# Kernel tuning notes

Hardware: AMD Instinct MI355X
Metric: run time of the kernel (lower is better)

Reference implementation:

```python
import jax, jax.numpy as jnp
import numpy as np

N = 100000   # nodes
E = 1600000  # directed edges
F_IN = 100
H = 256
N_LABELS = 19
BN_EPS = 1e-5


def setup_inputs() -> dict:
    key = jax.random.key(0)
    ks = jax.random.split(key, 12)
    p = lambda k, shape, s=0.05: jax.random.normal(k, shape, dtype=jnp.float32) * s
    return {
        "x": jax.random.normal(ks[0], (N, F_IN), dtype=jnp.float32),
        "edge_index": jax.random.randint(ks[1], (2, E), 0, N, dtype=jnp.int32),
        "W1": p(ks[2], (F_IN, F_IN)), "b1": jnp.zeros((F_IN,), jnp.float32),
        "W2": p(ks[3], (F_IN, F_IN)), "b2": jnp.zeros((F_IN,), jnp.float32),
        "W3": p(ks[4], (F_IN, H)),   "b3": jnp.zeros((H,), jnp.float32),
        "fc1_W": p(ks[5], (H, H)),   "fc1_b": jnp.zeros((H,), jnp.float32),
        "fc2a_W": p(ks[6], (H, 128)), "fc2a_b": jnp.zeros((128,), jnp.float32),
        "bn_gamma": jnp.ones((128,), jnp.float32), "bn_beta": jnp.zeros((128,), jnp.float32),
        "fc2b_W": p(ks[7], (128, N_LABELS)), "fc2b_b": jnp.zeros((N_LABELS,), jnp.float32),
    }


def _gcn_conv(x, W, b, src, dst, dinv):
    """PyG GCNConv with add_self_loops + symmetric normalization.
    out[dst] += dinv[src]*dinv[dst] * (x @ W)[src], plus self-loop term, plus bias.
    """
    n = x.shape[0]
    xw = x @ W  # [N, out]
    norm = dinv[src] * dinv[dst]  # [E]
    agg = jax.ops.segment_sum(xw[src] * norm[:, None], dst, num_segments=n)
    agg = agg + xw * (dinv * dinv)[:, None]  # self loops (i -> i)
    return agg + b


def reference(x, edge_index, W1, b1, W2, b2, W3, b3, fc1_W, fc1_b,
              fc2a_W, fc2a_b, bn_gamma, bn_beta, fc2b_W, fc2b_b):
    src, dst = edge_index[0], edge_index[1]
    n = x.shape[0]
    # degree of augmented graph (A + I), computed on targets (sum aggregation)
    deg = jax.ops.segment_sum(jnp.ones((src.shape[0],), x.dtype), dst, num_segments=n) + 1.0
    dinv = jax.lax.rsqrt(deg)

    h = jnp.clip(x, -0.4, 0.4)
    h = jax.nn.relu(_gcn_conv(h, W1, b1, src, dst, dinv))
    h = jax.nn.relu(_gcn_conv(h, W2, b2, src, dst, dinv))
    h = jax.nn.relu(_gcn_conv(h, W3, b3, src, dst, dinv))
    h = jax.nn.relu(h @ fc1_W + fc1_b)
    # fc2: Linear -> BatchNorm1d (train mode, batch stats) -> ReLU -> Linear
    h = h @ fc2a_W + fc2a_b
    mu = jnp.mean(h, axis=0)
    var = jnp.mean(jnp.square(h - mu), axis=0)  # biased var, as torch BN uses
    h = (h - mu) * jax.lax.rsqrt(var + BN_EPS) * bn_gamma + bn_beta
    h = jax.nn.relu(h)
    logits = h @ fc2b_W + fc2b_b
    return jax.nn.log_softmax(logits, axis=1)
```

## Files before the change

kernel.cpp:

```cpp
#include <hip/hip_runtime.h>
#include <hip/hip_bf16.h>

#define N_NODES 100000
#define N_EDGES 1600000
#define F_IN_DIM 100
#define F_IN_PAD 104
#define H_DIM 256
#define BN_DIM 128
#define N_LABELS 19
#define BN_EPS 1e-5f

#define BUCKET_SHIFT 8
#define NB 391
#define EPB 4096
#define PB 391

typedef __attribute__((ext_vector_type(8))) short bf16x8;
typedef __attribute__((ext_vector_type(4))) short s16x4;
typedef __attribute__((ext_vector_type(4))) float f32x4;

static __device__ inline short f2bf(float f) {
    __hip_bfloat16 h = __float2bfloat16(f);
    return *(short*)&h;
}
static __device__ inline float bf2f(short s) {
    unsigned u = ((unsigned)(unsigned short)s) << 16;
    return __builtin_bit_cast(float, u);
}

__global__ __launch_bounds__(256) void part_hist_kernel(const int* __restrict__ dst,
                                                        int* __restrict__ part_hist, int E)
{
    __shared__ int h[NB];
    int tid = threadIdx.x;
    for (int i = tid; i < NB; i += 256) h[i] = 0;
    __syncthreads();
    int base = blockIdx.x * EPB;
    int end = min(base + EPB, E);
    for (int e = base + tid; e < end; e += 256)
        atomicAdd(&h[dst[e] >> BUCKET_SHIFT], 1);
    __syncthreads();
    for (int i = tid; i < NB; i += 256) part_hist[blockIdx.x * NB + i] = h[i];
}

__global__ __launch_bounds__(512) void bucket_total_kernel(const int* __restrict__ part_hist,
                                                           int* __restrict__ bucket_total)
{
    __shared__ int ls[512];
    int b = blockIdx.x;
    int s = 0;
    for (int p = threadIdx.x; p < PB; p += 512) s += part_hist[p * NB + b];
    ls[threadIdx.x] = s;
    __syncthreads();
    for (int off = 256; off > 0; off >>= 1) {
        if (threadIdx.x < off) ls[threadIdx.x] += ls[threadIdx.x + off];
        __syncthreads();
    }
    if (threadIdx.x == 0) bucket_total[b] = ls[0];
}

__global__ __launch_bounds__(512) void bucket_scan_kernel(const int* __restrict__ bucket_total,
                                                          int* __restrict__ bucket_base)
{
    __shared__ int ls[512];
    int tid = threadIdx.x;
    ls[tid] = (tid < NB) ? bucket_total[tid] : 0;
    __syncthreads();
    for (int off = 1; off < 512; off <<= 1) {
        int v = ls[tid];
        int add = (tid >= off) ? ls[tid - off] : 0;
        __syncthreads();
        ls[tid] = v + add;
        __syncthreads();
    }
    if (tid < NB) bucket_base[tid] = (tid > 0) ? ls[tid - 1] : 0;
    if (tid == 0) bucket_base[NB] = ls[NB - 1];
}

__global__ __launch_bounds__(512) void part_offset_kernel(int* __restrict__ part_hist,
                                                          const int* __restrict__ bucket_base)
{
    __shared__ int ls[512];
    int b = blockIdx.x;
    int tid = threadIdx.x;
    int v = (tid < PB) ? part_hist[tid * NB + b] : 0;
    ls[tid] = v;
    __syncthreads();
    for (int off = 1; off < 512; off <<= 1) {
        int x = ls[tid];
        int add = (tid >= off) ? ls[tid - off] : 0;
        __syncthreads();
        ls[tid] = x + add;
        __syncthreads();
    }
    if (tid < PB) part_hist[tid * NB + b] = bucket_base[b] + ((tid > 0) ? ls[tid - 1] : 0);
}

__global__ __launch_bounds__(256) void partition_kernel(const int* __restrict__ src,
                                                        const int* __restrict__ dst,
                                                        const int* __restrict__ part_hist,
                                                        int* __restrict__ ep, int E)
{
    __shared__ int cur[NB];
    int tid = threadIdx.x;
    for (int i = tid; i < NB; i += 256) cur[i] = part_hist[blockIdx.x * NB + i];
    __syncthreads();
    int base = blockIdx.x * EPB;
    int end = min(base + EPB, E);
    for (int e = base + tid; e < end; e += 256) {
        int d = dst[e];
        int s = src[e];
        int pos = atomicAdd(&cur[d >> BUCKET_SHIFT], 1);
        ep[pos] = (s << 8) | (d & 255);
    }
}

__global__ __launch_bounds__(256) void bucket_csr_kernel(const int* __restrict__ ep,
                                                         const int* __restrict__ bucket_base,
                                                         int* __restrict__ row_start,
                                                         float* __restrict__ dinv,
                                                         int* __restrict__ src_sorted, int N, int E)
{
    __shared__ int h[256], sc[256], cur[256];
    int b = blockIdx.x;
    int tid = threadIdx.x;
    int e0 = bucket_base[b], e1 = bucket_base[b + 1];
    int node0 = b << BUCKET_SHIFT;
    int nn = min(256, N - node0);

    h[tid] = 0;
    __syncthreads();
    for (int e = e0 + tid; e < e1; e += 256)
        atomicAdd(&h[ep[e] & 255], 1);
    __syncthreads();

    sc[tid] = h[tid];
    __syncthreads();
    for (int off = 1; off < 256; off <<= 1) {
        int v = sc[tid];
        int add = (tid >= off) ? sc[tid - off] : 0;
        __syncthreads();
        sc[tid] = v + add;
        __syncthreads();
    }
    int excl = e0 + ((tid > 0) ? sc[tid - 1] : 0);
    if (tid < nn) {
        row_start[node0 + tid] = excl;
        dinv[node0 + tid] = rsqrtf((float)h[tid] + 1.0f);
    }
    cur[tid] = excl;
    __syncthreads();
    for (int e = e0 + tid; e < e1; e += 256) {
        int p = ep[e];
        int pos = atomicAdd(&cur[p & 255], 1);
        src_sorted[pos] = ((unsigned)p) >> 8;
    }
    if (b == 0 && tid == 0) row_start[N] = E;
}

__global__ __launch_bounds__(256) void pack_all(
    const float* __restrict__ W1, const float* __restrict__ W2, const float* __restrict__ W3,
    const float* __restrict__ Wf1, const float* __restrict__ Wf2a,
    short* __restrict__ Wt1, short* __restrict__ Wt2, short* __restrict__ Wt3,
    short* __restrict__ Wtf1, short* __restrict__ Wtf2a)
{
    int idx = blockIdx.x * 256 + threadIdx.x;
    const float* W; short* Wt; int K, N, Kp, local;
    if (idx < 10400)       { W = W1;   Wt = Wt1;   K = 100; N = 100; Kp = 104; local = idx; }
    else if (idx < 20800)  { W = W2;   Wt = Wt2;   K = 100; N = 100; Kp = 104; local = idx - 10400; }
    else if (idx < 47424)  { W = W3;   Wt = Wt3;   K = 100; N = 256; Kp = 104; local = idx - 20800; }
    else if (idx < 112960) { W = Wf1;  Wt = Wtf1;  K = 256; N = 256; Kp = 256; local = idx - 47424; }
    else if (idx < 145728) { W = Wf2a; Wt = Wtf2a; K = 256; N = 128; Kp = 256; local = idx - 112960; }
    else return;
    int n = local / Kp, k = local - n * Kp;
    Wt[local] = (k < K) ? f2bf(W[(size_t)k * N + n]) : (short)0;
}

template<int ABF16>
__global__ __launch_bounds__(256) void gemm_oneshot(
    const void* __restrict__ Av, const short* __restrict__ Wt,
    const float* __restrict__ bias, const float* __restrict__ rowscale,
    short* __restrict__ C, int M, int Nout, int strideA, int strideC, int relu)
{
    __shared__ __align__(16) short As[128][F_IN_PAD];
    __shared__ __align__(16) short Bs[128][F_IN_PAD];
    int tid = threadIdx.x;
    int rowBase = blockIdx.x * 128;
    int colBase = blockIdx.y * 128;

    if (ABF16) {
        const short* A = (const short*)Av;
        for (int ch = tid; ch < 128 * 13; ch += 256) {
            int r = ch / 13, c8 = (ch - r * 13) * 8;
            int gr = rowBase + r;
            bf16x8 o = (bf16x8){0,0,0,0,0,0,0,0};
            if (gr < M) o = *(const bf16x8*)(A + (size_t)gr * strideA + c8);
            *(bf16x8*)(&As[r][c8]) = o;
        }
    } else {
        const float* A = (const float*)Av;
        for (int ch = tid; ch < 128 * 25; ch += 256) {
            int r = ch / 25, c4 = (ch - r * 25) * 4;
            int gr = rowBase + r;
            float4 v = make_float4(0.f, 0.f, 0.f, 0.f);
            if (gr < M) v = *(const float4*)(A + (size_t)gr * strideA + c4);
            v.x = fminf(fmaxf(v.x, -0.4f), 0.4f);
            v.y = fminf(fmaxf(v.y, -0.4f), 0.4f);
            v.z = fminf(fmaxf(v.z, -0.4f), 0.4f);
            v.w = fminf(fmaxf(v.w, -0.4f), 0.4f);
            s16x4 o = (s16x4){f2bf(v.x), f2bf(v.y), f2bf(v.z), f2bf(v.w)};
            *(s16x4*)(&As[r][c4]) = o;
        }
        for (int r = tid; r < 128; r += 256)
            *(s16x4*)(&As[r][100]) = (s16x4){0, 0, 0, 0};
    }
    for (int ch = tid; ch < 128 * 13; ch += 256) {
        int n = ch / 13, c8 = (ch - n * 13) * 8;
        int gn = colBase + n;
        bf16x8 o = (bf16x8){0,0,0,0,0,0,0,0};
        if (gn < Nout) o = *(const bf16x8*)(Wt + (size_t)gn * F_IN_PAD + c8);
        *(bf16x8*)(&Bs[n][c8]) = o;
    }
    __syncthreads();

    int wid = tid >> 6;
    int lane = tid & 63;
    int quad = lane >> 4, l15 = lane & 15;
    int wave_m = (wid & 1) * 64;
    int wave_n = (wid >> 1) * 64;

    f32x4 acc[4][4];
    #pragma unroll
    for (int i = 0; i < 4; i++)
        #pragma unroll
        for (int j = 0; j < 4; j++)
            acc[i][j] = (f32x4){0.f, 0.f, 0.f, 0.f};

    #pragma unroll
    for (int kc = 0; kc < 4; kc++) {
        int off = kc * 32 + quad * 8;
        bool ok = (off + 8 <= F_IN_PAD);
        bf16x8 a[4], b[4];
        #pragma unroll
        for (int im = 0; im < 4; im++)
            a[im] = ok ? *(const bf16x8*)(&As[wave_m + im * 16 + l15][off])
                       : (bf16x8){0,0,0,0,0,0,0,0};
        #pragma unroll
        for (int in = 0; in < 4; in++)
            b[in] = ok ? *(const bf16x8*)(&Bs[wave_n + in * 16 + l15][off])
                       : (bf16x8){0,0,0,0,0,0,0,0};
        #pragma unroll
        for (int im = 0; im < 4; im++)
            #pragma unroll
            for (int in = 0; in < 4; in++)
                acc[im][in] = __builtin_amdgcn_mfma_f32_16x16x32_bf16(
                    a[im], b[in], acc[im][in], 0, 0, 0);
    }

    #pragma unroll
    for (int im = 0; im < 4; im++) {
        #pragma unroll
        for (int reg = 0; reg < 4; reg++) {
            int row = rowBase + wave_m + im * 16 + quad * 4 + reg;
            if (row >= M) continue;
            float rs = rowscale ? rowscale[row] : 1.f;
            #pragma unroll
            for (int in = 0; in < 4; in++) {
                int col = colBase + wave_n + in * 16 + l15;
                if (col >= strideC) continue;
                float v = 0.f;
                if (col < Nout) {
                    v = acc[im][in][reg];
                    if (bias) v += bias[col];
                    v *= rs;
                    if (relu) v = fmaxf(v, 0.f);
                }
                C[(size_t)row * strideC + col] = f2bf(v);
            }
        }
    }
}

#define SAP 72
__global__ __launch_bounds__(256) void gemm_mfma(
    const short* __restrict__ A, const short* __restrict__ Wt,
    const float* __restrict__ bias, const float* __restrict__ rowscale,
    short* __restrict__ C, int M, int Kp, int Nout,
    int strideA, int strideC, int relu)
{
    __shared__ __align__(16) short As[128][SAP];
    __shared__ __align__(16) short Bs[128][SAP];

    int tid = threadIdx.x;
    int wid = tid >> 6;
    int lane = tid & 63;
    int quad = lane >> 4;
    int l15 = lane & 15;
    int wave_m = (wid & 1) * 64;
    int wave_n = (wid >> 1) * 64;
    int rowBase = blockIdx.y * 128;
    int colBase = blockIdx.x * 128;

    f32x4 acc[4][4];
    #pragma unroll
    for (int i = 0; i < 4; i++)
        #pragma unroll
        for (int j = 0; j < 4; j++)
            acc[i][j] = (f32x4){0.f, 0.f, 0.f, 0.f};

    bf16x8 pa[4], pb[4];
    int nIter = (Kp + 63) >> 6;

    auto loadA = [&](int k0) {
        #pragma unroll
        for (int i = 0; i < 4; i++) {
            int ch = tid + i * 256;
            int r = ch >> 3, c8 = (ch & 7) << 3;
            int gr = rowBase + r, gk = k0 + c8;
            bf16x8 o = (bf16x8){0,0,0,0,0,0,0,0};
            if (gr < M && gk < strideA)
                o = *(const bf16x8*)(A + (size_t)gr * strideA + gk);
            pa[i] = o;
        }
    };
    auto loadB = [&](int k0) {
        #pragma unroll
        for (int i = 0; i < 4; i++) {
            int ch = tid + i * 256;
            int n = ch >> 3, c8 = (ch & 7) << 3;
            int gn = colBase + n, gk = k0 + c8;
            bf16x8 o = (bf16x8){0,0,0,0,0,0,0,0};
            if (gn < Nout && gk < Kp)
                o = *(const bf16x8*)(Wt + (size_t)gn * Kp + gk);
            pb[i] = o;
        }
    };
    auto storeAB = [&]() {
        #pragma unroll
        for (int i = 0; i < 4; i++) {
            int ch = tid + i * 256;
            int r = ch >> 3, c8 = (ch & 7) << 3;
            *(bf16x8*)(&As[r][c8]) = pa[i];
            *(bf16x8*)(&Bs[r][c8]) = pb[i];
        }
    };

    loadA(0); loadB(0);
    for (int it = 0; it < nIter; ++it) {
        if (it > 0) __syncthreads();
        storeAB();
        __syncthreads();
        if (it + 1 < nIter) { loadA((it + 1) << 6); loadB((it + 1) << 6); }
        #pragma unroll
        for (int ks = 0; ks < 2; ks++) {
            bf16x8 a[4], b[4];
            #pragma unroll
            for (int im = 0; im < 4; im++)
                a[im] = *(const bf16x8*)(&As[wave_m + im * 16 + l15][quad * 8 + ks * 32]);
            #pragma unroll
            for (int in = 0; in < 4; in++)
                b[in] = *(const bf16x8*)(&Bs[wave_n + in * 16 + l15][quad * 8 + ks * 32]);
            #pragma unroll
            for (int im = 0; im < 4; im++)
                #pragma unroll
                for (int in = 0; in < 4; in++)
                    acc[im][in] = __builtin_amdgcn_mfma_f32_16x16x32_bf16(
                        a[im], b[in], acc[im][in], 0, 0, 0);
        }
    }

    #pragma unroll
    for (int im = 0; im < 4; im++) {
        #pragma unroll
        for (int reg = 0; reg < 4; reg++) {
            int row = rowBase + wave_m + im * 16 + quad * 4 + reg;
            if (row >= M) continue;
            float rs = rowscale ? rowscale[row] : 1.f;
            #pragma unroll
            for (int in = 0; in < 4; in++) {
                int col = colBase + wave_n + in * 16 + l15;
                if (col >= strideC) continue;
                float v = 0.f;
                if (col < Nout) {
                    v = acc[im][in][reg];
                    if (bias) v += bias[col];
                    v *= rs;
                    if (relu) v = fmaxf(v, 0.f);
                }
                C[(size_t)row * strideC + col] = f2bf(v);
            }
        }
    }
}

template<int F, int STRIDE, int T, int MODE>
__global__ void gather_kernel(const short* __restrict__ xws,
                              const int* __restrict__ row_start,
                              const int* __restrict__ src_sorted,
                              const float* __restrict__ dinv,
                              const float* __restrict__ bias,
                              short* __restrict__ out, int n)
{
    constexpr int CHUNKS = STRIDE / 8;
    int group = (blockIdx.x * blockDim.x + threadIdx.x) / T;
    int lane = threadIdx.x % T;
    if (group >= n) return;
    int d = group;
    int e0 = row_start[d], e1 = row_start[d + 1];
    bool active = (lane < CHUNKS);
    int coff = lane * 8;
    float acc[8] = {};
    for (int e = e0; e < e1; e++) {
        int s = src_sorted[e];
        if (active) {
            bf16x8 v = *(const bf16x8*)(xws + (size_t)s * STRIDE + coff);
            #pragma unroll
            for (int j = 0; j < 8; j++) acc[j] += bf2f(v[j]);
        }
    }
    if (active) {
        bf16x8 xv = *(const bf16x8*)(xws + (size_t)d * STRIDE + coff);
        float di = dinv[d];
        bf16x8 o;
        #pragma unroll
        for (int j = 0; j < 8; j++) {
            int col = coff + j;
            float v = 0.f;
            if (col < F) {
                v = di * (acc[j] + bf2f(xv[j]));
                if (MODE == 0) v = fmaxf(v + bias[col], 0.f);
                if (MODE == 1) v = di * fmaxf(v + bias[col], 0.f);
            }
            o[j] = f2bf(v);
        }
        *(bf16x8*)(out + (size_t)d * STRIDE + coff) = o;
    }
}

__global__ void bn_stats_kernel(const short* __restrict__ h,
                                float* __restrict__ sum, float* __restrict__ sumsq, int Ntot)
{
    int c = threadIdx.x & 127;
    int rpb = blockDim.x >> 7;
    int r0 = blockIdx.x * rpb + (threadIdx.x >> 7);
    int stride = gridDim.x * rpb;
    float s = 0.f, ss = 0.f;
    for (int r = r0; r < Ntot; r += stride) {
        float v = bf2f(h[(size_t)r * BN_DIM + c]);
        s += v; ss += v * v;
    }
    __shared__ float ls[256], lss[256];
    ls[threadIdx.x] = s; lss[threadIdx.x] = ss;
    __syncthreads();
    if (threadIdx.x < 128) {
        s = ls[threadIdx.x] + ls[threadIdx.x + 128];
        ss = lss[threadIdx.x] + lss[threadIdx.x + 128];
        atomicAdd(&sum[c], s);
        atomicAdd(&sumsq[c], ss);
    }
}

__global__ void bn_finalize_kernel(const float* __restrict__ sum, const float* __restrict__ sumsq,
                                   const float* __restrict__ gamma, const float* __restrict__ beta,
                                   float* __restrict__ a, float* __restrict__ b, int Ntot)
{
    int c = threadIdx.x;
    float inv_n = 1.0f / (float)Ntot;
    float mu = sum[c] * inv_n;
    float var = sumsq[c] * inv_n - mu * mu;
    float ai = gamma[c] * rsqrtf(var + BN_EPS);
    a[c] = ai;
    b[c] = beta[c] - mu * ai;
}

__global__ __launch_bounds__(256) void fc2b_fused_kernel(
    const short* __restrict__ h, const float* __restrict__ bn_a, const float* __restrict__ bn_b,
    const float* __restrict__ W, const float* __restrict__ bias,
    float* __restrict__ out, int Ntot)
{
    __shared__ float Ws[BN_DIM][N_LABELS + 1];
    __shared__ float as[BN_DIM], bs[BN_DIM];
    for (int i = threadIdx.x; i < BN_DIM * N_LABELS; i += 256) {
        int k = i / N_LABELS, j = i - k * N_LABELS;
        Ws[k][j] = W[i];
    }
    if (threadIdx.x < BN_DIM) {
        as[threadIdx.x] = bn_a[threadIdx.x];
        bs[threadIdx.x] = bn_b[threadIdx.x];
    }
    __syncthreads();

    int r = blockIdx.x * 256 + threadIdx.x;
    if (r >= Ntot) return;

    float acc[N_LABELS];
    #pragma unroll
    for (int j = 0; j < N_LABELS; j++) acc[j] = bias[j];

    const short* hr = h + (size_t)r * BN_DIM;
    #pragma unroll
    for (int k0 = 0; k0 < BN_DIM; k0 += 8) {
        bf16x8 hv = *(const bf16x8*)(hr + k0);
        #pragma unroll
        for (int t = 0; t < 8; t++) {
            float v = fmaxf(bf2f(hv[t]) * as[k0 + t] + bs[k0 + t], 0.f);
            #pragma unroll
            for (int j = 0; j < N_LABELS; j++)
                acc[j] = fmaf(v, Ws[k0 + t][j], acc[j]);
        }
    }

    float m = acc[0];
    #pragma unroll
    for (int j = 1; j < N_LABELS; j++) m = fmaxf(m, acc[j]);
    float s = 0.f;
    #pragma unroll
    for (int j = 0; j < N_LABELS; j++) s += expf(acc[j] - m);
    float lse = m + logf(s);
    float* o = out + (size_t)r * N_LABELS;
    #pragma unroll
    for (int j = 0; j < N_LABELS; j++) o[j] = acc[j] - lse;
}

extern "C" void kernel_launch(void* const* d_in, const int* in_sizes, int n_in,
                              void* d_out, int out_size, void* d_ws, size_t ws_size,
                              hipStream_t stream)
{
    const float* x      = (const float*)d_in[0];
    const int*   ei     = (const int*)d_in[1];
    const float* W1     = (const float*)d_in[2];
    const float* b1     = (const float*)d_in[3];
    const float* W2     = (const float*)d_in[4];
    const float* b2     = (const float*)d_in[5];
    const float* W3     = (const float*)d_in[6];
    const float* b3     = (const float*)d_in[7];
    const float* fc1_W  = (const float*)d_in[8];
    const float* fc1_b  = (const float*)d_in[9];
    const float* fc2aW  = (const float*)d_in[10];
    const float* fc2ab  = (const float*)d_in[11];
    const float* gamma  = (const float*)d_in[12];
    const float* beta   = (const float*)d_in[13];
    const float* fc2bW  = (const float*)d_in[14];
    const float* fc2bb  = (const float*)d_in[15];
    float* out = (float*)d_out;

    const int* src = ei;
    const int* dst = ei + N_EDGES;

    char* w = (char*)d_ws;
    float* dinv        = (float*)w;  w += ((size_t)N_NODES * 4 + 255) / 256 * 256;
    int*   row_start   = (int*)w;    w += ((size_t)(N_NODES + 1) * 4 + 255) / 256 * 256;
    int*   part_hist   = (int*)w;    w += ((size_t)PB * NB * 4 + 255) / 256 * 256;
    int*   bucket_total= (int*)w;    w += ((size_t)NB * 4 + 255) / 256 * 256;
    int*   bucket_base = (int*)w;    w += ((size_t)(NB + 1) * 4 + 255) / 256 * 256;
    float* bn_sum      = (float*)w;  w += 128 * 4;
    float* bn_sumsq    = (float*)w;  w += 128 * 4;
    float* bn_a        = (float*)w;  w += 128 * 4;
    float* bn_b        = (float*)w;  w += 128 * 4;
    short* Wt1         = (short*)w;  w += ((size_t)F_IN_DIM * F_IN_PAD * 2 + 255) / 256 * 256;
    short* Wt2         = (short*)w;  w += ((size_t)F_IN_DIM * F_IN_PAD * 2 + 255) / 256 * 256;
    short* Wt3         = (short*)w;  w += ((size_t)H_DIM * F_IN_PAD * 2 + 255) / 256 * 256;
    short* Wtf1        = (short*)w;  w += ((size_t)H_DIM * H_DIM * 2 + 255) / 256 * 256;
    short* Wtf2a       = (short*)w;  w += ((size_t)BN_DIM * H_DIM * 2 + 255) / 256 * 256;
    int*   src_sorted  = (int*)w;    w += ((size_t)N_EDGES * 4 + 255) / 256 * 256;
    int*   ep          = (int*)w;    w += ((size_t)N_EDGES * 4 + 255) / 256 * 256;
    short* xws100      = (short*)w;  w += ((size_t)N_NODES * F_IN_PAD * 2 + 255) / 256 * 256;
    short* agg100      = (short*)w;  w += ((size_t)N_NODES * F_IN_PAD * 2 + 255) / 256 * 256;
    short* big1        = (short*)w;  w += ((size_t)N_NODES * H_DIM * 2 + 255) / 256 * 256;
    short* big2        = (short*)w;  w += ((size_t)N_NODES * H_DIM * 2 + 255) / 256 * 256;

    part_hist_kernel<<<PB, 256, 0, stream>>>(dst, part_hist, N_EDGES);
    bucket_total_kernel<<<NB, 512, 0, stream>>>(part_hist, bucket_total);
    bucket_scan_kernel<<<1, 512, 0, stream>>>(bucket_total, bucket_base);
    part_offset_kernel<<<NB, 512, 0, stream>>>(part_hist, bucket_base);
    partition_kernel<<<PB, 256, 0, stream>>>(src, dst, part_hist, ep, N_EDGES);
    bucket_csr_kernel<<<NB, 256, 0, stream>>>(ep, bucket_base, row_start, dinv,
                                              src_sorted, N_NODES, N_EDGES);

    pack_all<<<570, 256, 0, stream>>>(W1, W2, W3, fc1_W, fc2aW, Wt1, Wt2, Wt3, Wtf1, Wtf2a);

    const int nOne = (N_NODES + 127) / 128;
    int gatherBlocks = (N_NODES * 16 + 255) / 256;

    gemm_oneshot<0><<<dim3(nOne, 1), 256, 0, stream>>>(
        x, Wt1, nullptr, dinv, xws100, N_NODES, F_IN_DIM, F_IN_DIM, F_IN_PAD, 0);
    gather_kernel<F_IN_DIM, F_IN_PAD, 16, 0><<<gatherBlocks, 256, 0, stream>>>(
        xws100, row_start, src_sorted, dinv, b1, agg100, N_NODES);

    gemm_oneshot<1><<<dim3(nOne, 1), 256, 0, stream>>>(
        agg100, Wt2, nullptr, dinv, xws100, N_NODES, F_IN_DIM, F_IN_PAD, F_IN_PAD, 0);
    gather_kernel<F_IN_DIM, F_IN_PAD, 16, 1><<<gatherBlocks, 256, 0, stream>>>(
        xws100, row_start, src_sorted, dinv, b2, agg100, N_NODES);

    gather_kernel<F_IN_DIM, F_IN_PAD, 16, 2><<<gatherBlocks, 256, 0, stream>>>(
        agg100, row_start, src_sorted, dinv, nullptr, xws100, N_NODES);
    gemm_oneshot<1><<<dim3(nOne, 2), 256, 0, stream>>>(
        xws100, Wt3, b3, nullptr, big1, N_NODES, H_DIM, F_IN_PAD, H_DIM, 1);

    gemm_mfma<<<dim3(2, nOne), 256, 0, stream>>>(
        big1, Wtf1, fc1_b, nullptr, big2, N_NODES, H_DIM, H_DIM, H_DIM, H_DIM, 1);

    gemm_mfma<<<dim3(1, nOne), 256, 0, stream>>>(
        big2, Wtf2a, fc2ab, nullptr, big1, N_NODES, H_DIM, BN_DIM, H_DIM, BN_DIM, 0);

    hipMemsetAsync(bn_sum, 0, 2 * 128 * 4, stream);
    bn_stats_kernel<<<512, 256, 0, stream>>>(big1, bn_sum, bn_sumsq, N_NODES);
    bn_finalize_kernel<<<1, 128, 0, stream>>>(bn_sum, bn_sumsq, gamma, beta, bn_a, bn_b, N_NODES);

    fc2b_fused_kernel<<<(N_NODES + 255) / 256, 256, 0, stream>>>(
        big1, bn_a, bn_b, fc2bW, fc2bb, out, N_NODES);
}
```

Before: 725.3 us.

## Replace pipelined 128x128 GEMM with one-shot K=256 64x64 tile kernel

The two dense layers with K=256 (fc1 and fc2a) now use a new kernel that loads a whole 64-row by 256-K A tile and a 64-column B tile into shared memory in one go. It uses an XOR swizzle to avoid bank conflicts and drops the double-buffered K loop and its repeated barriers. Smaller tiles give more blocks and better occupancy, but A rows are reloaded once per column tile (4x for fc1, 2x for fc2a), so global reads rise. Each wave computes only a 64x16 output slice, which lowers register use but also MFMA work per LDS read.

```diff
diff --git a/kernel.cpp b/kernel.cpp
--- a/kernel.cpp
+++ b/kernel.cpp
@@ -281,114 +281,74 @@
     }
 }
 
-#define SAP 72
-__global__ __launch_bounds__(256) void gemm_mfma(
+__global__ __launch_bounds__(256) void gemm_oneshot256(
     const short* __restrict__ A, const short* __restrict__ Wt,
-    const float* __restrict__ bias, const float* __restrict__ rowscale,
-    short* __restrict__ C, int M, int Kp, int Nout,
-    int strideA, int strideC, int relu)
-{
-    __shared__ __align__(16) short As[128][SAP];
-    __shared__ __align__(16) short Bs[128][SAP];
-
-    int tid = threadIdx.x;
-    int wid = tid >> 6;
+    const float* __restrict__ bias, short* __restrict__ C,
+    int M, int Nout, int strideC, int relu)
+{
+    __shared__ __align__(16) short As[64 * 256];
+    __shared__ __align__(16) short Bs[64 * 256];
+    int tid = threadIdx.x;
+    int rowBase = blockIdx.x * 64;
+    int colBase = blockIdx.y * 64;
+
+    #pragma unroll
+    for (int i = 0; i < 8; i++) {
+        int ch = tid + i * 256;
+        int r = ch >> 5, c = ch & 31;
+        int gr = rowBase + r;
+        bf16x8 o = (bf16x8){0,0,0,0,0,0,0,0};
+        if (gr < M) o = *(const bf16x8*)(A + (size_t)gr * 256 + (c << 3));
+        *(bf16x8*)(&As[(r << 8) + (((c ^ r) & 31) << 3)]) = o;
+    }
+    #pragma unroll
+    for (int i = 0; i < 8; i++) {
+        int ch = tid + i * 256;
+        int n = ch >> 5, c = ch & 31;
+        int gn = colBase + n;
+        bf16x8 o = (bf16x8){0,0,0,0,0,0,0,0};
+        if (gn < Nout) o = *(const bf16x8*)(Wt + (size_t)gn * 256 + (c << 3));
+        *(bf16x8*)(&Bs[(n << 8) + (((c ^ n) & 31) << 3)]) = o;
+    }
+    __syncthreads();
+
+    int wv = tid >> 6;
     int lane = tid & 63;
-    int quad = lane >> 4;
-    int l15 = lane & 15;
-    int wave_m = (wid & 1) * 64;
-    int wave_n = (wid >> 1) * 64;
-    int rowBase = blockIdx.y * 128;
-    int colBase = blockIdx.x * 128;
-
-    f32x4 acc[4][4];
-    #pragma unroll
-    for (int i = 0; i < 4; i++)
-        #pragma unroll
-        for (int j = 0; j < 4; j++)
-            acc[i][j] = (f32x4){0.f, 0.f, 0.f, 0.f};
-
-    bf16x8 pa[4], pb[4];
-    int nIter = (Kp + 63) >> 6;
-
-    auto loadA = [&](int k0) {
-        #pragma unroll
-        for (int i = 0; i < 4; i++) {
-            int ch = tid + i * 256;
-            int r = ch >> 3, c8 = (ch & 7) << 3;
-            int gr = rowBase + r, gk = k0 + c8;
-            bf16x8 o = (bf16x8){0,0,0,0,0,0,0,0};
-            if (gr < M && gk < strideA)
-                o = *(const bf16x8*)(A + (size_t)gr * strideA + gk);
-            pa[i] = o;
-        }
-    };
-    auto loadB = [&](int k0) {
-        #pragma unroll
-        for (int i = 0; i < 4; i++) {
-            int ch = tid + i * 256;
-            int n = ch >> 3, c8 = (ch & 7) << 3;
-            int gn = colBase + n, gk = k0 + c8;
-            bf16x8 o = (bf16x8){0,0,0,0,0,0,0,0};
-            if (gn < Nout && gk < Kp)
-                o = *(const bf16x8*)(Wt + (size_t)gn * Kp + gk);
-            pb[i] = o;
-        }
-    };
-    auto storeAB = [&]() {
-        #pragma unroll
-        for (int i = 0; i < 4; i++) {
-            int ch = tid + i * 256;
-            int r = ch >> 3, c8 = (ch & 7) << 3;
-            *(bf16x8*)(&As[r][c8]) = pa[i];
-            *(bf16x8*)(&Bs[r][c8]) = pb[i];
-        }
-    };
-
-    loadA(0); loadB(0);
-    for (int it = 0; it < nIter; ++it) {
-        if (it > 0) __syncthreads();
-        storeAB();
-        __syncthreads();
-        if (it + 1 < nIter) { loadA((it + 1) << 6); loadB((it + 1) << 6); }
-        #pragma unroll
-        for (int ks = 0; ks < 2; ks++) {
-            bf16x8 a[4], b[4];
-            #pragma unroll
-            for (int im = 0; im < 4; im++)
-                a[im] = *(const bf16x8*)(&As[wave_m + im * 16 + l15][quad * 8 + ks * 32]);
-            #pragma unroll
-            for (int in = 0; in < 4; in++)
-                b[in] = *(const bf16x8*)(&Bs[wave_n + in * 16 + l15][quad * 8 + ks * 32]);
-            #pragma unroll
-            for (int im = 0; im < 4; im++)
-                #pragma unroll
-                for (int in = 0; in < 4; in++)
-                    acc[im][in] = __builtin_amdgcn_mfma_f32_16x16x32_bf16(
-                        a[im], b[in], acc[im][in], 0, 0, 0);
-        }
-    }
-
+    int quad = lane >> 4, l15 = lane & 15;
+    int ncol = wv * 16 + l15;
+
+    f32x4 acc[4];
+    #pragma unroll
+    for (int im = 0; im < 4; im++) acc[im] = (f32x4){0.f, 0.f, 0.f, 0.f};
+
+    #pragma unroll
+    for (int kc = 0; kc < 8; kc++) {
+        int c0 = kc * 4 + quad;
+        bf16x8 b = *(const bf16x8*)(&Bs[(ncol << 8) + (((c0 ^ ncol) & 31) << 3)]);
+        #pragma unroll
+        for (int im = 0; im < 4; im++) {
+            int mrow = im * 16 + l15;
+            bf16x8 a = *(const bf16x8*)(&As[(mrow << 8) + (((c0 ^ mrow) & 31) << 3)]);
+            acc[im] = __builtin_amdgcn_mfma_f32_16x16x32_bf16(a, b, acc[im], 0, 0, 0);
+        }
+    }
+
+    int col = colBase + ncol;
+    bool cvalid = col < Nout;
+    float bv = (bias && cvalid) ? bias[col] : 0.f;
     #pragma unroll
     for (int im = 0; im < 4; im++) {
         #pragma unroll
         for (int reg = 0; reg < 4; reg++) {
-            int row = rowBase + wave_m + im * 16 + quad * 4 + reg;
+            int row = rowBase + im * 16 + quad * 4 + reg;
             if (row >= M) continue;
-            float rs = rowscale ? rowscale[row] : 1.f;
-            #pragma unroll
-            for (int in = 0; in < 4; in++) {
-                int col = colBase + wave_n + in * 16 + l15;
-                if (col >= strideC) continue;
-                float v = 0.f;
-                if (col < Nout) {
-                    v = acc[im][in][reg];
-                    if (bias) v += bias[col];
-                    v *= rs;
-                    if (relu) v = fmaxf(v, 0.f);
-                }
+            float v = 0.f;
+            if (cvalid) {
+                v = acc[im][reg] + bv;
+                if (relu) v = fmaxf(v, 0.f);
+            }
+            if (col < strideC)
                 C[(size_t)row * strideC + col] = f2bf(v);
-            }
         }
     }
 }
@@ -580,6 +540,7 @@
     pack_all<<<570, 256, 0, stream>>>(W1, W2, W3, fc1_W, fc2aW, Wt1, Wt2, Wt3, Wtf1, Wtf2a);
 
     const int nOne = (N_NODES + 127) / 128;
+    const int n64  = (N_NODES + 63) / 64;
     int gatherBlocks = (N_NODES * 16 + 255) / 256;
 
     gemm_oneshot<0><<<dim3(nOne, 1), 256, 0, stream>>>(
@@ -597,11 +558,11 @@
     gemm_oneshot<1><<<dim3(nOne, 2), 256, 0, stream>>>(
         xws100, Wt3, b3, nullptr, big1, N_NODES, H_DIM, F_IN_PAD, H_DIM, 1);
 
-    gemm_mfma<<<dim3(2, nOne), 256, 0, stream>>>(
-        big1, Wtf1, fc1_b, nullptr, big2, N_NODES, H_DIM, H_DIM, H_DIM, H_DIM, 1);
-
-    gemm_mfma<<<dim3(1, nOne), 256, 0, stream>>>(
-        big2, Wtf2a, fc2ab, nullptr, big1, N_NODES, H_DIM, BN_DIM, H_DIM, BN_DIM, 0);
+    gemm_oneshot256<<<dim3(n64, 4), 256, 0, stream>>>(
+        big1, Wtf1, fc1_b, big2, N_NODES, H_DIM, H_DIM, 1);
+
+    gemm_oneshot256<<<dim3(n64, 2), 256, 0, stream>>>(
+        big2, Wtf2a, fc2ab, big1, N_NODES, BN_DIM, BN_DIM, 0);
 
     hipMemsetAsync(bn_sum, 0, 2 * 128 * 4, stream);
     bn_stats_kernel<<<512, 256, 0, stream>>>(big1, bn_sum, bn_sumsq, N_NODES);
```

New measurement: 759.6 us. 4.7% more time.

## Add one-shot full-K MFMA GEMM for fc1 and unroll gather edge loop by two

Applied to the files above, without the earlier changes.

Adds a gemm_oneshot256 kernel that loads a full 64x256 A tile and a 64x256 weight tile into XOR-swizzled LDS once, then runs all K steps with 16x16x32 bf16 MFMA and no K-loop synchronisation. fc1 now uses it instead of the tiled gemm_mfma kernel. This removes per-K-tile barriers and may help LDS bank conflicts, but uses 64KB of LDS per block, which can limit occupancy, and reloads A once per column block. Separately, the gather loop processes two edges per iteration so that more independent loads are in flight.

```diff
diff --git a/kernel.cpp b/kernel.cpp
--- a/kernel.cpp
+++ b/kernel.cpp
@@ -281,6 +281,78 @@
     }
 }
 
+__global__ __launch_bounds__(256) void gemm_oneshot256(
+    const short* __restrict__ A, const short* __restrict__ Wt,
+    const float* __restrict__ bias, short* __restrict__ C,
+    int M, int Nout, int strideC, int relu)
+{
+    __shared__ __align__(16) short As[64 * 256];
+    __shared__ __align__(16) short Bs[64 * 256];
+    int tid = threadIdx.x;
+    int rowBase = blockIdx.y * 64;
+    int colBase = blockIdx.x * 64;
+
+    #pragma unroll
+    for (int i = 0; i < 8; i++) {
+        int ch = tid + i * 256;
+        int r = ch >> 5, c = ch & 31;
+        int gr = rowBase + r;
+        bf16x8 o = (bf16x8){0,0,0,0,0,0,0,0};
+        if (gr < M) o = *(const bf16x8*)(A + (size_t)gr * 256 + (c << 3));
+        *(bf16x8*)(&As[(r << 8) + (((c ^ r) & 31) << 3)]) = o;
+    }
+    #pragma unroll
+    for (int i = 0; i < 8; i++) {
+        int ch = tid + i * 256;
+        int n = ch >> 5, c = ch & 31;
+        int gn = colBase + n;
+        bf16x8 o = (bf16x8){0,0,0,0,0,0,0,0};
+        if (gn < Nout) o = *(const bf16x8*)(Wt + (size_t)gn * 256 + (c << 3));
+        *(bf16x8*)(&Bs[(n << 8) + (((c ^ n) & 31) << 3)]) = o;
+    }
+    __syncthreads();
+
+    int wv = tid >> 6;
+    int lane = tid & 63;
+    int quad = lane >> 4, l15 = lane & 15;
+    int ncol = wv * 16 + l15;
+
+    f32x4 acc[4];
+    #pragma unroll
+    for (int im = 0; im < 4; im++) acc[im] = (f32x4){0.f, 0.f, 0.f, 0.f};
+
+    #pragma unroll
+    for (int kc = 0; kc < 8; kc++) {
+        int c0 = kc * 4 + quad;
+        bf16x8 b = *(const bf16x8*)(&Bs[(ncol << 8) + (((c0 ^ ncol) & 31) << 3)]);
+        #pragma unroll
+        for (int im = 0; im < 4; im++) {
+            int mrow = im * 16 + l15;
+            bf16x8 a = *(const bf16x8*)(&As[(mrow << 8) + (((c0 ^ mrow) & 31) << 3)]);
+            acc[im] = __builtin_amdgcn_mfma_f32_16x16x32_bf16(a, b, acc[im], 0, 0, 0);
+        }
+    }
+
+    int col = colBase + ncol;
+    bool cvalid = col < Nout;
+    float bv = (bias && cvalid) ? bias[col] : 0.f;
+    #pragma unroll
+    for (int im = 0; im < 4; im++) {
+        #pragma unroll
+        for (int reg = 0; reg < 4; reg++) {
+            int row = rowBase + im * 16 + quad * 4 + reg;
+            if (row >= M) continue;
+            float v = 0.f;
+            if (cvalid) {
+                v = acc[im][reg] + bv;
+                if (relu) v = fmaxf(v, 0.f);
+            }
+            if (col < strideC)
+                C[(size_t)row * strideC + col] = f2bf(v);
+        }
+    }
+}
+
 #define SAP 72
 __global__ __launch_bounds__(256) void gemm_mfma(
     const short* __restrict__ A, const short* __restrict__ Wt,
@@ -410,7 +482,17 @@
     bool active = (lane < CHUNKS);
     int coff = lane * 8;
     float acc[8] = {};
-    for (int e = e0; e < e1; e++) {
+    int e = e0;
+    for (; e + 1 < e1; e += 2) {
+        int s0 = src_sorted[e], s1 = src_sorted[e + 1];
+        if (active) {
+            bf16x8 v0 = *(const bf16x8*)(xws + (size_t)s0 * STRIDE + coff);
+            bf16x8 v1 = *(const bf16x8*)(xws + (size_t)s1 * STRIDE + coff);
+            #pragma unroll
+            for (int j = 0; j < 8; j++) acc[j] += bf2f(v0[j]) + bf2f(v1[j]);
+        }
+    }
+    if (e < e1) {
         int s = src_sorted[e];
         if (active) {
             bf16x8 v = *(const bf16x8*)(xws + (size_t)s * STRIDE + coff);
@@ -580,6 +662,7 @@
     pack_all<<<570, 256, 0, stream>>>(W1, W2, W3, fc1_W, fc2aW, Wt1, Wt2, Wt3, Wtf1, Wtf2a);
 
     const int nOne = (N_NODES + 127) / 128;
+    const int n64  = (N_NODES + 63) / 64;
     int gatherBlocks = (N_NODES * 16 + 255) / 256;
 
     gemm_oneshot<0><<<dim3(nOne, 1), 256, 0, stream>>>(
@@ -597,8 +680,8 @@
     gemm_oneshot<1><<<dim3(nOne, 2), 256, 0, stream>>>(
         xws100, Wt3, b3, nullptr, big1, N_NODES, H_DIM, F_IN_PAD, H_DIM, 1);
 
-    gemm_mfma<<<dim3(2, nOne), 256, 0, stream>>>(
-        big1, Wtf1, fc1_b, nullptr, big2, N_NODES, H_DIM, H_DIM, H_DIM, H_DIM, 1);
+    gemm_oneshot256<<<dim3(4, n64), 256, 0, stream>>>(
+        big1, Wtf1, fc1_b, big2, N_NODES, H_DIM, H_DIM, 1);
 
     gemm_mfma<<<dim3(1, nOne), 256, 0, stream>>>(
         big2, Wtf2a, fc2ab, nullptr, big1, N_NODES, H_DIM, BN_DIM, H_DIM, BN_DIM, 0);
```

After: 785.5 us. +8.3%, slower.
